# Kernel tuning notes

Measured on AMD Instinct MI355X. Metric: run time of the kernel, lower is better.

## Reference

```python
import jax, jax.numpy as jnp
import numpy as np

B, D, L, H = 4, 1024, 2048, 16
Dh = D // H
SCALE = np.sqrt(Dh).astype(np.float32)


def setup_inputs() -> dict:
    key = jax.random.key(0)
    ks = jax.random.split(key, 6)
    s = 1.0 / np.sqrt(D)
    return {
        "x": jax.random.normal(ks[0], (B, D, 1, L), dtype=jnp.float32),
        "wq": jax.random.normal(ks[1], (D, D), dtype=jnp.float32) * s,
        "wk": jax.random.normal(ks[2], (D, D), dtype=jnp.float32) * s,
        "wv": jax.random.normal(ks[3], (D, D), dtype=jnp.float32) * s,
        "wo": jax.random.normal(ks[4], (D, D), dtype=jnp.float32) * s,
        "bo": jax.random.normal(ks[5], (D,), dtype=jnp.float32) * 0.01,
    }


def reference(x, wq, wk, wv, wo, bo):
    # x: (B, D, 1, L) -> (B, D, L); 1x1 conv == channel matmul
    xc = x[:, :, 0, :]  # (B, D, L)
    q = jnp.einsum('od,bdl->bol', wq, xc).reshape(B, H, Dh, L)
    k = jnp.einsum('od,bdl->bol', wk, xc).reshape(B, H, Dh, L)
    v = jnp.einsum('od,bdl->bol', wv, xc).reshape(B, H, Dh, L)
    attn = jnp.einsum('bhdi,bhdj->bhij', q, k) / SCALE  # (B,H,L,L)
    attn = jax.nn.softmax(attn, axis=-1)  # dropout is identity at eval
    out = jnp.einsum('bhij,bhdj->bhdi', attn, v).reshape(B, D, L)
    out = jnp.einsum('od,bdl->bol', wo, out) + bo[None, :, None]
    return out[:, :, None, :]  # (B, D, 1, L)
```

## Files before the change

kernel.cpp:

```cpp
#include <hip/hip_runtime.h>
#include <math.h>

#define NB 4
#define ND 1024
#define NL 2048
#define NH 16
#define NDH 64

typedef float f4 __attribute__((ext_vector_type(4)));
typedef float f32x4 __attribute__((ext_vector_type(4)));
typedef short bf16x8 __attribute__((ext_vector_type(8)));
typedef unsigned short u16;
typedef u16 u16x4 __attribute__((ext_vector_type(4)));
typedef unsigned long long u64;

#define MFMA16 __builtin_amdgcn_mfma_f32_16x16x32_bf16

__device__ __forceinline__ u16 bf16_rne(float f) {
  unsigned u = __float_as_uint(f);
  u += 0x7fffu + ((u >> 16) & 1u);
  return (u16)(u >> 16);
}
__device__ __forceinline__ float bf16_to_f(u16 h) {
  return __uint_as_float(((unsigned)h) << 16);
}
__device__ __forceinline__ unsigned cvt_pk_bf16(float a, float b) {
  unsigned r;
  asm("v_cvt_pk_bf16_f32 %0, %1, %2" : "=v"(r) : "v"(a), "v"(b));
  return r;
}
__device__ __forceinline__ void gll16(const void* g, void* l) {
  __builtin_amdgcn_global_load_lds(
      (const __attribute__((address_space(1))) void*)g,
      (__attribute__((address_space(3))) void*)l, 16, 0, 0);
}

__global__ __launch_bounds__(256) void prep_x(const float* __restrict__ X,
                                              u16* __restrict__ Xhi,
                                              u16* __restrict__ Xlo) {
  __shared__ float t[64][65];
  const int tid = threadIdx.x;
  const int l0 = blockIdx.x * 64, d0 = blockIdx.y * 64, b = blockIdx.z;
  const float* Xb = X + ((size_t)b * ND + d0) * NL + l0;
#pragma unroll
  for (int r = 0; r < 16; ++r) {
    int idx = tid + r * 256;
    int d = idx >> 6, l = idx & 63;
    t[d][l] = Xb[(size_t)d * NL + l];
  }
  __syncthreads();
#pragma unroll
  for (int r = 0; r < 16; ++r) {
    int idx = tid + r * 256;
    int li = idx >> 6, dd = idx & 63;
    float v = t[dd][li];
    u16 hh = bf16_rne(v);
    size_t o = ((size_t)b * NL + l0 + li) * ND + d0 + dd;
    Xhi[o] = hh;
    Xlo[o] = bf16_rne(v - bf16_to_f(hh));
  }
}

__global__ __launch_bounds__(256) void prep_w(const float* __restrict__ W,
                                              u16* __restrict__ Whi,
                                              u16* __restrict__ Wlo) {
  int i = blockIdx.x * 256 + threadIdx.x;
  f4 v = ((const f4*)W)[i];
  u16x4 h, l;
#pragma unroll
  for (int k = 0; k < 4; ++k) {
    h[k] = bf16_rne(v[k]);
    l[k] = bf16_rne(v[k] - bf16_to_f(h[k]));
  }
  ((u16x4*)Whi)[i] = h;
  ((u16x4*)Wlo)[i] = l;
}

template <int MODE>
__global__ __launch_bounds__(256) void gemm_split(
    const u16* __restrict__ Ahi, const u16* __restrict__ Alo,
    const u16* __restrict__ Bhi, const u16* __restrict__ Blo,
    float* __restrict__ Cf, const float* __restrict__ bias,
    u16* __restrict__ Chi, u16* __restrict__ Clo, float scale) {
  __shared__ char smem[65536];
  const int tid = threadIdx.x;
  const int lane = tid & 63, wv = tid >> 6;
  const int l0 = blockIdx.x * 128, o0 = blockIdx.y * 128, b = blockIdx.z;
  const int wo = (wv >> 1) * 64, wl = (wv & 1) * 64;

  const int pr = tid >> 3;
  const int e = (tid & 7) ^ (pr & 7);
  const int r_src = pr * 2 + (e >> 2);
  const int s_src = e & 3;
  const char* gAh = (const char*)(Ahi + (size_t)(o0 + r_src) * ND) + s_src * 16;
  const char* gAl = (const char*)(Alo + (size_t)(o0 + r_src) * ND) + s_src * 16;
  const char* gBh = (const char*)(Bhi + ((size_t)b * NL + l0 + r_src) * ND) + s_src * 16;
  const char* gBl = (const char*)(Blo + ((size_t)b * NL + l0 + r_src) * ND) + s_src * 16;
  const int QROW = 64 * ND * 2;

  const int fswz = ((((lane & 1) << 2) | (lane >> 4)) ^ ((lane >> 1) & 7)) << 4;
  int offA[4], offB[4];
#pragma unroll
  for (int f = 0; f < 4; ++f) {
    offA[f] = ((wo + 16 * f + (lane & 15)) >> 1) * 128 + fswz;
    offB[f] = ((wl + 16 * f + (lane & 15)) >> 1) * 128 + fswz;
  }

  f32x4 acc[4][4];
#pragma unroll
  for (int mf = 0; mf < 4; ++mf)
#pragma unroll
    for (int nf = 0; nf < 4; ++nf) acc[mf][nf] = 0.0f;

  auto stage = [&](char* bb, int kbyte) {
    char* d = bb + wv * 1024;
    gll16(gAh + kbyte, d);
    gll16(gAh + kbyte + QROW, d + 4096);
    gll16(gAl + kbyte, d + 8192);
    gll16(gAl + kbyte + QROW, d + 12288);
    gll16(gBh + kbyte, d + 16384);
    gll16(gBh + kbyte + QROW, d + 20480);
    gll16(gBl + kbyte, d + 24576);
    gll16(gBl + kbyte + QROW, d + 28672);
  };

  stage(smem, 0);
  int cur = 0;
  for (int ks = 0; ks < ND / 32; ++ks) {
    __syncthreads();
    if (ks + 1 < ND / 32) stage(smem + (cur ^ 1) * 32768, (ks + 1) * 64);
    const char* sb = smem + cur * 32768;
    bf16x8 ah[4], al[4], bh[4], bl[4];
#pragma unroll
    for (int f = 0; f < 4; ++f) {
      ah[f] = *(const bf16x8*)(sb + offA[f]);
      al[f] = *(const bf16x8*)(sb + 8192 + offA[f]);
      bh[f] = *(const bf16x8*)(sb + 16384 + offB[f]);
      bl[f] = *(const bf16x8*)(sb + 24576 + offB[f]);
    }
    __builtin_amdgcn_s_setprio(1);
#pragma unroll
    for (int mf = 0; mf < 4; ++mf)
#pragma unroll
      for (int nf = 0; nf < 4; ++nf) {
        acc[mf][nf] = MFMA16(ah[mf], bh[nf], acc[mf][nf], 0, 0, 0);
        acc[mf][nf] = MFMA16(ah[mf], bl[nf], acc[mf][nf], 0, 0, 0);
        acc[mf][nf] = MFMA16(al[mf], bh[nf], acc[mf][nf], 0, 0, 0);
      }
    __builtin_amdgcn_s_setprio(0);
    cur ^= 1;
  }

  const int col = lane & 15, row4 = (lane >> 4) * 4;
  if constexpr (MODE == 0) {
    const size_t cb = (size_t)b * ND * NL;
#pragma unroll
    for (int mf = 0; mf < 4; ++mf)
#pragma unroll
      for (int rg = 0; rg < 4; ++rg) {
        int o = o0 + wo + 16 * mf + row4 + rg;
        float bv = bias[o];
        float* crow = Cf + cb + (size_t)o * NL + l0 + wl + col;
#pragma unroll
        for (int nf = 0; nf < 4; ++nf) crow[16 * nf] = acc[mf][nf][rg] + bv;
      }
  } else if constexpr (MODE == 1) {
#pragma unroll
    for (int nf = 0; nf < 4; ++nf) {
      size_t lrow = ((size_t)b * NL + l0 + wl + 16 * nf + col) * ND + o0 + wo;
#pragma unroll
      for (int mf = 0; mf < 4; ++mf) {
        u16x4 h, l;
#pragma unroll
        for (int rg = 0; rg < 4; ++rg) {
          float v = acc[mf][nf][rg] * scale;
          h[rg] = bf16_rne(v);
          l[rg] = bf16_rne(v - bf16_to_f(h[rg]));
        }
        *(u16x4*)(Chi + lrow + 16 * mf + row4) = h;
        *(u16x4*)(Clo + lrow + 16 * mf + row4) = l;
      }
    }
  } else {
    const size_t cb = (size_t)b * ND * NL;
#pragma unroll
    for (int mf = 0; mf < 4; ++mf)
#pragma unroll
      for (int rg = 0; rg < 4; ++rg) {
        int o = o0 + wo + 16 * mf + row4 + rg;
        u16* hrow = Chi + cb + (size_t)o * NL + l0 + wl + col;
#pragma unroll
        for (int nf = 0; nf < 4; ++nf) {
          float v = acc[mf][nf][rg];
          hrow[16 * nf] = bf16_rne(v);
        }
        if (Clo) {
          u16* lrow2 = Clo + cb + (size_t)o * NL + l0 + wl + col;
#pragma unroll
          for (int nf = 0; nf < 4; ++nf) {
            float v = acc[mf][nf][rg];
            lrow2[16 * nf] = bf16_rne(v - bf16_to_f(bf16_rne(v)));
          }
        }
      }
  }
}

__global__ __launch_bounds__(256) void attn_mfma(
    const u16* __restrict__ Qh, const u16* __restrict__ Ql,
    const u16* __restrict__ Kh, const u16* __restrict__ Kl,
    const u16* __restrict__ Vh,
    u16* __restrict__ Oh, u16* __restrict__ Ol) {
  __shared__ char smem[65536];
  const int tid = threadIdx.x, lane = tid & 63, wv = tid >> 6;
  const int il = lane & 15, g = lane >> 4, x7 = il & 7;
  const int i0 = blockIdx.x * 128, h = blockIdx.y, b = blockIdx.z;
  const int iw = i0 + wv * 32;

  bf16x8 qh[2][2], ql[2][2];
  {
#pragma unroll
    for (int mf = 0; mf < 2; ++mf) {
      size_t rowq = ((size_t)b * NL + iw + 16 * mf + il) * ND + h * NDH + g * 8;
#pragma unroll
      for (int ks = 0; ks < 2; ++ks) {
        qh[mf][ks] = *(const bf16x8*)(Qh + rowq + ks * 32);
        ql[mf][ks] = *(const bf16x8*)(Ql + rowq + ks * 32);
      }
    }
  }

  const int r0 = tid >> 3;
  const int swz0 = ((tid & 7) ^ (r0 & 7)) << 4;
  const char* gKh = (const char*)(Kh + ((size_t)b * NL + r0) * ND + h * NDH) + swz0;
  const char* gKl = (const char*)(Kl + ((size_t)b * NL + r0) * ND + h * NDH) + swz0;
  const char* gVh = (const char*)(Vh + ((size_t)b * ND + h * NDH + r0) * NL) + swz0;
  const int RSK = 32 * ND * 2, RSV = 32 * NL * 2;
  const int BUF = 24576, PBASE = 49152;

  auto stage = [&](char* bb, int jt) {
    char* d = bb + wv * 1024;
    int ka = jt * (64 * ND * 2);
    int va = jt * 128;
    gll16(gKh + ka, d);
    gll16(gKh + ka + RSK, d + 4096);
    gll16(gKl + ka, d + 8192);
    gll16(gKl + ka + RSK, d + 12288);
    gll16(gVh + va, d + 16384);
    gll16(gVh + va + RSV, d + 20480);
  };

  int slotb[2];
#pragma unroll
  for (int ks = 0; ks < 2; ++ks) slotb[ks] = (((ks << 2) + g) ^ x7) << 4;
  const int frow = il * 128;
  int prow[2];
#pragma unroll
  for (int mf = 0; mf < 2; ++mf)
    prow[mf] = PBASE + (wv * 32 + mf * 16 + il) * 128;

  f32x4 ot[4][2];
  float mrow[2], lrow[2];
#pragma unroll
  for (int df = 0; df < 4; ++df)
#pragma unroll
    for (int mf = 0; mf < 2; ++mf) ot[df][mf] = 0.0f;
  mrow[0] = mrow[1] = -INFINITY;
  lrow[0] = lrow[1] = 0.0f;

  stage(smem, 0);
  int cur = 0;
  for (int jt = 0; jt < NL / 64; ++jt) {
    __syncthreads();
    if (jt + 1 < NL / 64) stage(smem + (cur ^ 1) * BUF, jt + 1);
    const char* sb = smem + cur * BUF;

    f32x4 st[4][2];
#pragma unroll
    for (int jf = 0; jf < 4; ++jf)
#pragma unroll
      for (int mf = 0; mf < 2; ++mf) st[jf][mf] = 0.0f;
#pragma unroll
    for (int ks = 0; ks < 2; ++ks) {
#pragma unroll
      for (int jf = 0; jf < 4; ++jf) {
        int rb = jf * 2048 + frow + slotb[ks];
        bf16x8 kh = *(const bf16x8*)(sb + rb);
        bf16x8 kl = *(const bf16x8*)(sb + 8192 + rb);
        __builtin_amdgcn_s_setprio(1);
#pragma unroll
        for (int mf = 0; mf < 2; ++mf) {
          st[jf][mf] = MFMA16(kh, qh[mf][ks], st[jf][mf], 0, 0, 0);
          st[jf][mf] = MFMA16(kl, qh[mf][ks], st[jf][mf], 0, 0, 0);
          st[jf][mf] = MFMA16(kh, ql[mf][ks], st[jf][mf], 0, 0, 0);
        }
        __builtin_amdgcn_s_setprio(0);
      }
    }

    float alpha[2];
#pragma unroll
    for (int mf = 0; mf < 2; ++mf) {
      float mx = st[0][mf][0];
#pragma unroll
      for (int jf = 0; jf < 4; ++jf) {
        float a = fmaxf(st[jf][mf][0], st[jf][mf][1]);
        float c = fmaxf(st[jf][mf][2], st[jf][mf][3]);
        mx = fmaxf(mx, fmaxf(a, c));
      }
      mx = fmaxf(mx, __shfl_xor(mx, 16));
      mx = fmaxf(mx, __shfl_xor(mx, 32));
      float mo = mrow[mf];
      float mn = fmaxf(mo, mx);
      float al = __builtin_amdgcn_exp2f(mo - mn);
      mrow[mf] = mn;
      alpha[mf] = al;
      float sum = 0.0f;
#pragma unroll
      for (int jf = 0; jf < 4; ++jf) {
        float p0 = __builtin_amdgcn_exp2f(st[jf][mf][0] - mn);
        float p1 = __builtin_amdgcn_exp2f(st[jf][mf][1] - mn);
        float p2 = __builtin_amdgcn_exp2f(st[jf][mf][2] - mn);
        float p3 = __builtin_amdgcn_exp2f(st[jf][mf][3] - mn);
        sum += (p0 + p1) + (p2 + p3);
        unsigned w0 = cvt_pk_bf16(p0, p1);
        unsigned w1 = cvt_pk_bf16(p2, p3);
        int addr = prow[mf] + (((2 * jf + (g >> 1)) ^ x7) << 4) + ((g & 1) << 3);
        *(u64*)(smem + addr) = (u64)w0 | ((u64)w1 << 32);
      }
      sum += __shfl_xor(sum, 16);
      sum += __shfl_xor(sum, 32);
      lrow[mf] = al * lrow[mf] + sum;
    }

#pragma unroll
    for (int df = 0; df < 4; ++df)
#pragma unroll
      for (int mf = 0; mf < 2; ++mf)
#pragma unroll
        for (int rg = 0; rg < 4; ++rg) ot[df][mf][rg] *= alpha[mf];

#pragma unroll
    for (int ks = 0; ks < 2; ++ks) {
      bf16x8 pf[2];
#pragma unroll
      for (int mf = 0; mf < 2; ++mf)
        pf[mf] = *(const bf16x8*)(smem + prow[mf] + ((((ks << 2) + g) ^ x7) << 4));
#pragma unroll
      for (int df = 0; df < 4; ++df) {
        bf16x8 vh = *(const bf16x8*)(sb + 16384 + df * 2048 + frow + slotb[ks]);
        __builtin_amdgcn_s_setprio(1);
        ot[df][0] = MFMA16(vh, pf[0], ot[df][0], 0, 0, 0);
        ot[df][1] = MFMA16(vh, pf[1], ot[df][1], 0, 0, 0);
        __builtin_amdgcn_s_setprio(0);
      }
    }
    cur ^= 1;
  }

#pragma unroll
  for (int mf = 0; mf < 2; ++mf) {
    float linv = 1.0f / lrow[mf];
    size_t orow = ((size_t)b * NL + iw + 16 * mf + il) * ND + h * NDH;
#pragma unroll
    for (int df = 0; df < 4; ++df) {
      u16x4 hh, ll;
#pragma unroll
      for (int rg = 0; rg < 4; ++rg) {
        float v = ot[df][mf][rg] * linv;
        hh[rg] = bf16_rne(v);
        ll[rg] = bf16_rne(v - bf16_to_f(hh[rg]));
      }
      *(u16x4*)(Oh + orow + df * 16 + g * 4) = hh;
      *(u16x4*)(Ol + orow + df * 16 + g * 4) = ll;
    }
  }
}

extern "C" void kernel_launch(void* const* d_in, const int* in_sizes, int n_in,
                              void* d_out, int out_size, void* d_ws, size_t ws_size,
                              hipStream_t stream) {
  const float* x = (const float*)d_in[0];
  const float* wq = (const float*)d_in[1];
  const float* wk = (const float*)d_in[2];
  const float* wv = (const float*)d_in[3];
  const float* wo = (const float*)d_in[4];
  const float* bo = (const float*)d_in[5];
  float* out = (float*)d_out;

  const size_t EL = (size_t)NB * ND * NL;
  char* p = (char*)d_ws;
  u16* Xt_hi = (u16*)p; p += EL * 2;
  u16* Xt_lo = (u16*)p; p += EL * 2;
  u16* Qt_hi = (u16*)p; p += EL * 2;
  u16* Qt_lo = (u16*)p; p += EL * 2;
  u16* Kt_hi = (u16*)p; p += EL * 2;
  u16* Kt_lo = (u16*)p; p += EL * 2;
  u16* Vn_hi = (u16*)p; p += EL * 2;
  u16* Vn_lo = (u16*)p; p += EL * 2;
  const size_t WE = (size_t)ND * ND;
  u16 *Wh[4], *Wl[4];
  for (int i = 0; i < 4; ++i) {
    Wh[i] = (u16*)p; p += WE * 2;
    Wl[i] = (u16*)p; p += WE * 2;
  }
  u16* Ot_hi = Xt_hi;
  u16* Ot_lo = Xt_lo;

  dim3 tpb(256);
  prep_x<<<dim3(NL / 64, ND / 64, NB), tpb, 0, stream>>>(x, Xt_hi, Xt_lo);
  prep_w<<<dim3(WE / 1024), tpb, 0, stream>>>(wq, Wh[0], Wl[0]);
  prep_w<<<dim3(WE / 1024), tpb, 0, stream>>>(wk, Wh[1], Wl[1]);
  prep_w<<<dim3(WE / 1024), tpb, 0, stream>>>(wv, Wh[2], Wl[2]);
  prep_w<<<dim3(WE / 1024), tpb, 0, stream>>>(wo, Wh[3], Wl[3]);

  dim3 gg(NL / 128, ND / 128, NB);
  gemm_split<1><<<gg, tpb, 0, stream>>>(Wh[0], Wl[0], Xt_hi, Xt_lo, nullptr,
                                        nullptr, Qt_hi, Qt_lo,
                                        0.125f * 1.44269504088896f);
  gemm_split<1><<<gg, tpb, 0, stream>>>(Wh[1], Wl[1], Xt_hi, Xt_lo, nullptr,
                                        nullptr, Kt_hi, Kt_lo, 1.0f);
  gemm_split<2><<<gg, tpb, 0, stream>>>(Wh[2], Wl[2], Xt_hi, Xt_lo, nullptr,
                                        nullptr, Vn_hi, nullptr, 1.0f);

  attn_mfma<<<dim3(NL / 128, NH, NB), tpb, 0, stream>>>(
      Qt_hi, Qt_lo, Kt_hi, Kt_lo, Vn_hi, Ot_hi, Ot_lo);

  gemm_split<0><<<gg, tpb, 0, stream>>>(Wh[3], Wl[3], Ot_hi, Ot_lo, out, bo,
                                        nullptr, nullptr, 1.0f);
}
```

Before: 502.2 us.

## Keep P in registers via permlane swaps and defer softmax rescaling

Replaces the LDS round-trip for the softmax probability tile with in-register v_permlane32/16_swap shuffles that rebuild the MFMA B-operand fragments, and shrinks shared memory from 64KB to 48KB. Adds a wave-uniform lazy rescale: when the new row max stays within a threshold of the running max, the alpha rescale of the accumulator and row sum is skipped. This cuts LDS traffic and VALU work per tile and may raise occupancy. It adds cross-lane permute instructions and relies on the threshold keeping the exponentials from overflowing.

```diff
diff --git a/kernel.cpp b/kernel.cpp
--- a/kernel.cpp
+++ b/kernel.cpp
@@ -12,7 +12,6 @@
 typedef short bf16x8 __attribute__((ext_vector_type(8)));
 typedef unsigned short u16;
 typedef u16 u16x4 __attribute__((ext_vector_type(4)));
-typedef unsigned long long u64;
 
 #define MFMA16 __builtin_amdgcn_mfma_f32_16x16x32_bf16
 
@@ -211,7 +210,7 @@
     const u16* __restrict__ Kh, const u16* __restrict__ Kl,
     const u16* __restrict__ Vh,
     u16* __restrict__ Oh, u16* __restrict__ Ol) {
-  __shared__ char smem[65536];
+  __shared__ char smem[49152];
   const int tid = threadIdx.x, lane = tid & 63, wv = tid >> 6;
   const int il = lane & 15, g = lane >> 4, x7 = il & 7;
   const int i0 = blockIdx.x * 128, h = blockIdx.y, b = blockIdx.z;
@@ -236,7 +235,7 @@
   const char* gKl = (const char*)(Kl + ((size_t)b * NL + r0) * ND + h * NDH) + swz0;
   const char* gVh = (const char*)(Vh + ((size_t)b * ND + h * NDH + r0) * NL) + swz0;
   const int RSK = 32 * ND * 2, RSV = 32 * NL * 2;
-  const int BUF = 24576, PBASE = 49152;
+  const int BUF = 24576;
 
   auto stage = [&](char* bb, int jt) {
     char* d = bb + wv * 1024;
@@ -254,10 +253,6 @@
 #pragma unroll
   for (int ks = 0; ks < 2; ++ks) slotb[ks] = (((ks << 2) + g) ^ x7) << 4;
   const int frow = il * 128;
-  int prow[2];
-#pragma unroll
-  for (int mf = 0; mf < 2; ++mf)
-    prow[mf] = PBASE + (wv * 32 + mf * 16 + il) * 128;
 
   f32x4 ot[4][2];
   float mrow[2], lrow[2];
@@ -298,10 +293,10 @@
       }
     }
 
-    float alpha[2];
+    float mx2[2];
 #pragma unroll
     for (int mf = 0; mf < 2; ++mf) {
-      float mx = st[0][mf][0];
+      float mx = -INFINITY;
 #pragma unroll
       for (int jf = 0; jf < 4; ++jf) {
         float a = fmaxf(st[jf][mf][0], st[jf][mf][1]);
@@ -310,12 +305,27 @@
       }
       mx = fmaxf(mx, __shfl_xor(mx, 16));
       mx = fmaxf(mx, __shfl_xor(mx, 32));
-      float mo = mrow[mf];
-      float mn = fmaxf(mo, mx);
-      float al = __builtin_amdgcn_exp2f(mo - mn);
-      mrow[mf] = mn;
-      alpha[mf] = al;
+      mx2[mf] = mx;
+    }
+    const int defer =
+        __all((mx2[0] <= mrow[0] + 11.5f) && (mx2[1] <= mrow[1] + 11.5f));
+
+    bf16x8 pfrag[2][2];
+#pragma unroll
+    for (int mf = 0; mf < 2; ++mf) {
+      if (!defer) {
+        float mn = fmaxf(mrow[mf], mx2[mf]);
+        float al = __builtin_amdgcn_exp2f(mrow[mf] - mn);
+        mrow[mf] = mn;
+        lrow[mf] *= al;
+#pragma unroll
+        for (int df = 0; df < 4; ++df)
+#pragma unroll
+          for (int rg = 0; rg < 4; ++rg) ot[df][mf][rg] *= al;
+      }
+      const float mn = mrow[mf];
       float sum = 0.0f;
+      unsigned pk[4][2];
 #pragma unroll
       for (int jf = 0; jf < 4; ++jf) {
         float p0 = __builtin_amdgcn_exp2f(st[jf][mf][0] - mn);
@@ -323,35 +333,42 @@
         float p2 = __builtin_amdgcn_exp2f(st[jf][mf][2] - mn);
         float p3 = __builtin_amdgcn_exp2f(st[jf][mf][3] - mn);
         sum += (p0 + p1) + (p2 + p3);
-        unsigned w0 = cvt_pk_bf16(p0, p1);
-        unsigned w1 = cvt_pk_bf16(p2, p3);
-        int addr = prow[mf] + (((2 * jf + (g >> 1)) ^ x7) << 4) + ((g & 1) << 3);
-        *(u64*)(smem + addr) = (u64)w0 | ((u64)w1 << 32);
+        pk[jf][0] = cvt_pk_bf16(p0, p1);
+        pk[jf][1] = cvt_pk_bf16(p2, p3);
       }
       sum += __shfl_xor(sum, 16);
       sum += __shfl_xor(sum, 32);
-      lrow[mf] = al * lrow[mf] + sum;
-    }
-
-#pragma unroll
-    for (int df = 0; df < 4; ++df)
-#pragma unroll
-      for (int mf = 0; mf < 2; ++mf)
-#pragma unroll
-        for (int rg = 0; rg < 4; ++rg) ot[df][mf][rg] *= alpha[mf];
+      lrow[mf] += sum;
+
+#pragma unroll
+      for (int ks = 0; ks < 2; ++ks) {
+        unsigned u0, u1, u2, u3;
+        {
+          unsigned a = pk[2 * ks][0], bb2 = pk[2 * ks + 1][0];
+          asm volatile("v_permlane32_swap_b32 %0, %1" : "+v"(a), "+v"(bb2));
+          asm volatile("v_permlane16_swap_b32 %0, %1" : "+v"(a), "+v"(bb2));
+          u0 = a; u2 = bb2;
+        }
+        {
+          unsigned a = pk[2 * ks][1], bb2 = pk[2 * ks + 1][1];
+          asm volatile("v_permlane32_swap_b32 %0, %1" : "+v"(a), "+v"(bb2));
+          asm volatile("v_permlane16_swap_b32 %0, %1" : "+v"(a), "+v"(bb2));
+          u1 = a; u3 = bb2;
+        }
+        union { unsigned w[4]; bf16x8 v; } cv;
+        cv.w[0] = u0; cv.w[1] = u1; cv.w[2] = u2; cv.w[3] = u3;
+        pfrag[mf][ks] = cv.v;
+      }
+    }
 
 #pragma unroll
     for (int ks = 0; ks < 2; ++ks) {
-      bf16x8 pf[2];
-#pragma unroll
-      for (int mf = 0; mf < 2; ++mf)
-        pf[mf] = *(const bf16x8*)(smem + prow[mf] + ((((ks << 2) + g) ^ x7) << 4));
 #pragma unroll
       for (int df = 0; df < 4; ++df) {
         bf16x8 vh = *(const bf16x8*)(sb + 16384 + df * 2048 + frow + slotb[ks]);
         __builtin_amdgcn_s_setprio(1);
-        ot[df][0] = MFMA16(vh, pf[0], ot[df][0], 0, 0, 0);
-        ot[df][1] = MFMA16(vh, pf[1], ot[df][1], 0, 0, 0);
+        ot[df][0] = MFMA16(vh, pfrag[0][ks], ot[df][0], 0, 0, 0);
+        ot[df][1] = MFMA16(vh, pfrag[1][ks], ot[df][1], 0, 0, 0);
         __builtin_amdgcn_s_setprio(0);
       }
     }
```

Result: faster. 473.0 us (-5.8%).
